# Kernel tuning notes

Hardware: AMD Instinct MI355X
Metric: run time of the kernel (lower is better)

## Reference

```python
import jax, jax.numpy as jnp
import numpy as np

B, N, S, C_IN = 8, 1024, 64, 1
H = 32  # hidden_ch


def _mpnn(W, b, x, g):
    # Faithful to MPNN(concat_h=False): messages[b,c,m,n] = x[b,c,m] * g[b,n,m],
    # flattened to (c m) channels and hit by a 1x1 conv W of shape (H, c, m).
    # out[b,u,n] = sum_{c,m} W[u,c,m] * x[b,c,m] * g[b,n,m] + b[u]
    t = jnp.einsum('ucm,bcm->bum', W, x)          # tiny contraction over c
    return jnp.einsum('bum,bnm->bun', t, g) + b[None, :, None]


def setup_inputs() -> dict:
    key = jax.random.key(0)
    ks = jax.random.split(key, 14)
    gate_scale = 1.0 / np.sqrt(C_IN * N)

    def gate_w(k):
        return jax.random.normal(k, (H, C_IN, N), jnp.float32) * gate_scale

    return {
        'x': jax.random.normal(ks[0], (B, N, S, C_IN), jnp.float32),
        'mask': jnp.ones((B, N, S, C_IN), dtype=bool),  # unused by the module
        'fwd_graph': jax.random.uniform(ks[1], (B, N, N), jnp.float32),
        # GRU gate MPNN 1x1-conv weights, reshaped (H, C_IN*N, 1) -> (H, C_IN, N)
        'Wf': gate_w(ks[2]), 'bf': jnp.zeros((H,), jnp.float32),
        'Wu': gate_w(ks[3]), 'bu': jnp.zeros((H,), jnp.float32),
        'Wc': gate_w(ks[4]), 'bc': jnp.zeros((H,), jnp.float32),
        'h0': jnp.zeros((H, N), jnp.float32),
        'W1': jax.random.normal(ks[5], (H, H), jnp.float32) / np.sqrt(H),
        'b1': jnp.zeros((H,), jnp.float32),
        'W2': jax.random.normal(ks[6], (H, 2 * H), jnp.float32) / np.sqrt(2 * H),
        'b2': jnp.zeros((H,), jnp.float32),
        # LocalConv1D: per-node 1x1 conv, weights (n, out_ch, 2H), bias (n, out_ch)
        'Wd': jax.random.normal(ks[7], (N, C_IN, 2 * H), jnp.float32) / np.sqrt(2 * H),
        'bd': jnp.zeros((N, C_IN), jnp.float32),
    }


def reference(x, mask, fwd_graph, Wf, bf, Wu, bu, Wc, bc, h0, W1, b1, W2, b2, Wd, bd):
    del mask  # present in the torch signature but never used
    b = x.shape[0]
    xs = jnp.transpose(x, (2, 0, 3, 1))  # (s, b, c, n)
    g = fwd_graph
    h_init = jnp.broadcast_to(h0[None], (b, H, N))

    def step(h, x_t):
        # NOTE: with concat_h=False the forget gate r = sigmoid(MPNN_f(x)) only
        # rescales h passed into c_gate, which ignores h entirely -> r (Wf, bf)
        # has no effect on the output; omitted here (same math).
        u = jax.nn.sigmoid(_mpnn(Wu, bu, x_t, g))
        c = jnp.tanh(_mpnn(Wc, bc, x_t, g))
        h_new = u * h + (1.0 - u) * c
        return h_new, None

    h, _ = jax.lax.scan(step, h_init, xs)

    # Prediction head (only the last step's prediction is returned: pred[:, :, -1:])
    x1 = jax.nn.leaky_relu(jnp.einsum('uh,bhn->bun', W1, h) + b1[None, :, None])
    x2 = jax.nn.leaky_relu(
        jnp.einsum('uk,bkn->bun', W2, jnp.concatenate([x1, h], axis=1)) + b2[None, :, None])
    dec_in = jnp.concatenate([x2, h], axis=1)  # (b, 2H, n)
    # LocalConv1D (per-node weights), fully batched:
    x_hat = jnp.einsum('nok,bkn->bon', Wd, dec_in) + bd.T[None, :, :]  # (b, c, n)
    return jnp.transpose(x_hat, (0, 2, 1))[:, :, None, :]  # (b, n, 1, c)
```

## Files before the change

kernel.cpp:

```cpp
#include <hip/hip_runtime.h>
#include <hip/hip_bf16.h>
#include <hip/hip_fp16.h>

#define Bsz 8
#define Nn 1024
#define Ss 64
#define Hh 32

typedef _Float16 half8 __attribute__((ext_vector_type(8)));
typedef _Float16 half4 __attribute__((ext_vector_type(4)));
typedef float f32x4 __attribute__((ext_vector_type(4)));

__device__ __forceinline__ void gload_lds16(const _Float16* g, _Float16* l) {
  __builtin_amdgcn_global_load_lds(
      (const __attribute__((address_space(1))) unsigned int*)g,
      (__attribute__((address_space(3))) unsigned int*)l, 16, 0, 0);
}

__global__ __launch_bounds__(256)
void prep(const float* __restrict__ x, const float* __restrict__ Wu,
          const float* __restrict__ Wc, const float* __restrict__ g,
          _Float16* __restrict__ xT, _Float16* __restrict__ Wh,
          _Float16* __restrict__ gh) {
  const int tid = threadIdx.x;
  if (blockIdx.x < 64) {
    const int b = blockIdx.x >> 3;
    const int m0 = (blockIdx.x & 7) * 128;
    __shared__ _Float16 tile[128 * 68];
    const int m = tid >> 1;
    const int hf = tid & 1;
    const float* src = x + ((size_t)(b * Nn + m0 + m)) * Ss + hf * 32;
#pragma unroll
    for (int i = 0; i < 8; ++i) {
      const float4 v = *(const float4*)(src + i * 4);
      half4 o;
      o[0] = (_Float16)v.x; o[1] = (_Float16)v.y;
      o[2] = (_Float16)v.z; o[3] = (_Float16)v.w;
      *(half4*)(&tile[m * 68 + hf * 32 + i * 4]) = o;
    }
    __syncthreads();
    const int t = tid & 63;
    const int q = tid >> 6;
    _Float16* dst = xT + ((size_t)(b * 64 + t)) * Nn + m0 + q * 32;
#pragma unroll
    for (int i = 0; i < 4; ++i) {
      half8 o;
#pragma unroll
      for (int e = 0; e < 8; ++e) o[e] = tile[(q * 32 + i * 8 + e) * 68 + t];
      *(half8*)(dst + i * 8) = o;
    }
  } else if (blockIdx.x < 72) {
    const int w = blockIdx.x - 64;
    const size_t i0 = ((size_t)(w * 256 + tid)) * 32;
#pragma unroll
    for (int i = 0; i < 8; ++i) {
      const size_t i4 = i0 + i * 4;
      const float* s = (i4 < 32768) ? (Wu + i4) : (Wc + (i4 - 32768));
      const float4 v = *(const float4*)s;
      half4 o;
      o[0] = (_Float16)v.x; o[1] = (_Float16)v.y;
      o[2] = (_Float16)v.z; o[3] = (_Float16)v.w;
      *(half4*)(&Wh[i4]) = o;
    }
  } else {
    const size_t i = ((size_t)(blockIdx.x - 72) * 256 + tid) * 4;
    const float4 v = *(const float4*)(&g[i]);
    half4 o;
    o[0] = (_Float16)v.x; o[1] = (_Float16)v.y;
    o[2] = (_Float16)v.z; o[3] = (_Float16)v.w;
    *(half4*)(&gh[i]) = o;
  }
}

__global__ __launch_bounds__(256)
void gemm_recur(const _Float16* __restrict__ xT, const _Float16* __restrict__ Wh,
                const _Float16* __restrict__ G, const float* __restrict__ bu,
                const float* __restrict__ bc, const float* __restrict__ h0,
                float* __restrict__ H) {
  __shared__ __align__(16) char smem[12288];
  _Float16* Xs = (_Float16*)smem;
  _Float16* Gs = (_Float16*)(smem + 4096);

  const int id = blockIdx.x;
  const int wg = (id & 7) * 256 + (id >> 3);
  const int b = wg >> 8;
  const int u = wg & 31;
  const int col0 = ((wg >> 5) & 7) * 128;

  const int tid = threadIdx.x;
  const int lane = tid & 63;
  const int wave = tid >> 6;
  const int wc = wave * 32;
  const int l15 = lane & 15;
  const int s = lane >> 4;

  const _Float16* Xb = xT + (size_t)b * 64 * Nn;
  const _Float16* Gb = G + ((size_t)b * Nn + col0) * Nn;
  const _Float16* Wg0 = Wh + (size_t)u * Nn;
  const _Float16* Wg1 = Wh + (size_t)(32 + u) * Nn;

  const int srow = lane >> 2;
  const int ssw = ((lane & 3) ^ ((lane >> 3) & 3)) * 8;
  const int ps8 = (s ^ ((l15 >> 1) & 3)) * 8;

  f32x4 acc[8][2] = {};

  for (int kk = 0; kk < 32; ++kk) {
    const int k0 = kk * 32;
    gload_lds16(Xb + (size_t)(wave * 16 + srow) * Nn + k0 + ssw,
                Xs + wave * 512);
    gload_lds16(Gb + (size_t)(wave * 32 + srow) * Nn + k0 + ssw,
                Gs + wave * 1024);
    gload_lds16(Gb + (size_t)(wave * 32 + 16 + srow) * Nn + k0 + ssw,
                Gs + wave * 1024 + 512);
    const half8 wv0 = *(const half8*)(Wg0 + k0 + s * 8);
    const half8 wv1 = *(const half8*)(Wg1 + k0 + s * 8);
    __syncthreads();

    half8 xf[4], bf[2];
#pragma unroll
    for (int q = 0; q < 4; ++q)
      xf[q] = *(const half8*)(&Xs[(q * 16 + l15) * 32 + ps8]);
#pragma unroll
    for (int ni = 0; ni < 2; ++ni)
      bf[ni] = *(const half8*)(&Gs[(wc + ni * 16 + l15) * 32 + ps8]);
#pragma unroll
    for (int mi = 0; mi < 8; ++mi) {
      const half8 af = xf[mi & 3] * (mi < 4 ? wv0 : wv1);
#pragma unroll
      for (int ni = 0; ni < 2; ++ni)
        acc[mi][ni] = __builtin_amdgcn_mfma_f32_16x16x32_f16(af, bf[ni], acc[mi][ni], 0, 0, 0);
    }
    __syncthreads();
  }

  const float bias_u = bu[u];
  const float bias_c = bc[u];
#pragma unroll
  for (int ni = 0; ni < 2; ++ni) {
    float At = 1.f, Bt = 0.f;
#pragma unroll
    for (int mi = 0; mi < 4; ++mi) {
      float A = 1.f, B = 0.f;
#pragma unroll
      for (int j = 0; j < 4; ++j) {
        const float yu = acc[mi][ni][j] + bias_u;
        const float yc = acc[mi + 4][ni][j] + bias_c;
        const float ug = 1.f / (1.f + __expf(-yu));
        const float e = __expf(-2.f * fabsf(yc));
        float th = (1.f - e) / (1.f + e);
        th = yc < 0.f ? -th : th;
        const float bj = (1.f - ug) * th;
        B = ug * B + bj;
        A = ug * A;
      }
      float Aall = __shfl(A, l15, 64);
      float Ball = __shfl(B, l15, 64);
#pragma unroll
      for (int sp = 1; sp < 4; ++sp) {
        const float As = __shfl(A, sp * 16 + l15, 64);
        const float Bs = __shfl(B, sp * 16 + l15, 64);
        Ball = As * Ball + Bs;
        Aall = As * Aall;
      }
      Bt = Aall * Bt + Ball;
      At = Aall * At;
    }
    if (s == (ni << 1)) {
      const int n = col0 + wc + ni * 16 + l15;
      const float hv = At * h0[u * Nn + n] + Bt;
      H[((size_t)b * Hh + u) * Nn + n] = hv;
    }
  }
}

__global__ __launch_bounds__(128)
void head(const float* __restrict__ H, const float* __restrict__ W1,
          const float* __restrict__ b1, const float* __restrict__ W2,
          const float* __restrict__ b2, const float* __restrict__ Wd,
          const float* __restrict__ bd, float* __restrict__ out) {
  const int b = blockIdx.x >> 3;
  const int n = (blockIdx.x & 7) * 128 + threadIdx.x;
  const float* Hb = H + (size_t)b * Hh * Nn;
  float h[32];
#pragma unroll
  for (int u = 0; u < 32; ++u) h[u] = Hb[u * Nn + n];
  float x1[32];
#pragma unroll 4
  for (int v = 0; v < 32; ++v) {
    float a = b1[v];
#pragma unroll
    for (int u = 0; u < 32; ++u) a += W1[v * 32 + u] * h[u];
    x1[v] = a > 0.f ? a : 0.01f * a;
  }
  float x2[32];
#pragma unroll 4
  for (int v = 0; v < 32; ++v) {
    float a = b2[v];
#pragma unroll
    for (int u = 0; u < 32; ++u) a += W2[v * 64 + u] * x1[u];
#pragma unroll
    for (int u = 0; u < 32; ++u) a += W2[v * 64 + 32 + u] * h[u];
    x2[v] = a > 0.f ? a : 0.01f * a;
  }
  float o = bd[n];
#pragma unroll
  for (int v = 0; v < 32; ++v) o += Wd[n * 64 + v] * x2[v];
#pragma unroll
  for (int v = 0; v < 32; ++v) o += Wd[n * 64 + 32 + v] * h[v];
  out[(size_t)b * Nn + n] = o;
}

extern "C" void kernel_launch(void* const* d_in, const int* in_sizes, int n_in,
                              void* d_out, int out_size, void* d_ws, size_t ws_size,
                              hipStream_t stream) {
  const float* x  = (const float*)d_in[0];
  const float* g  = (const float*)d_in[2];
  const float* Wu = (const float*)d_in[5];
  const float* bu = (const float*)d_in[6];
  const float* Wc = (const float*)d_in[7];
  const float* bc = (const float*)d_in[8];
  const float* h0 = (const float*)d_in[9];
  const float* W1 = (const float*)d_in[10];
  const float* b1 = (const float*)d_in[11];
  const float* W2 = (const float*)d_in[12];
  const float* b2 = (const float*)d_in[13];
  const float* Wd = (const float*)d_in[14];
  const float* bd = (const float*)d_in[15];
  float* out = (float*)d_out;

  char* ws = (char*)d_ws;
  _Float16* xT = (_Float16*)(ws);
  _Float16* Wh = (_Float16*)(ws + (size_t)(1u << 20));
  _Float16* gh = (_Float16*)(ws + (size_t)(2u << 20));
  float*    Hx = (float*)  (ws + (size_t)(18u << 20));

  prep<<<72 + 8192, 256, 0, stream>>>(x, Wu, Wc, g, xT, Wh, gh);
  gemm_recur<<<2048, 256, 0, stream>>>(xT, Wh, gh, bu, bc, h0, Hx);
  head<<<64, 128, 0, stream>>>(Hx, W1, b1, W2, b2, Wd, bd, out);
}
```

Baseline: 225.7 us.

## Double-buffer LDS tiles with async prefetch and stage gate weights in LDS

Converts the K loop of the recurrence GEMM to a double-buffered pipeline. The next X/G tile is issued via global_load_lds before the current tile is computed, with manual vmcnt waits and raw s_barriers in place of two __syncthreads. The Wu/Wc rows are loaded once into LDS instead of from global memory every iteration. The weight scaling is moved from the X fragments (8 multiplies) to the G fragments (4 multiplies). LDS usage grows from 12 KB to 28 KB, which can lower occupancy, and the hand-written waitcnt logic is fragile.

```diff
diff --git a/kernel.cpp b/kernel.cpp
--- a/kernel.cpp
+++ b/kernel.cpp
@@ -77,9 +77,12 @@
                 const _Float16* __restrict__ G, const float* __restrict__ bu,
                 const float* __restrict__ bc, const float* __restrict__ h0,
                 float* __restrict__ H) {
-  __shared__ __align__(16) char smem[12288];
-  _Float16* Xs = (_Float16*)smem;
-  _Float16* Gs = (_Float16*)(smem + 4096);
+  __shared__ __align__(16) char smem[28672];
+  _Float16* X0 = (_Float16*)smem;
+  _Float16* G0 = (_Float16*)(smem + 4096);
+  _Float16* X1 = (_Float16*)(smem + 12288);
+  _Float16* G1 = (_Float16*)(smem + 16384);
+  _Float16* Ws = (_Float16*)(smem + 24576);
 
   const int id = blockIdx.x;
   const int wg = (id & 7) * 256 + (id >> 3);
@@ -96,8 +99,6 @@
 
   const _Float16* Xb = xT + (size_t)b * 64 * Nn;
   const _Float16* Gb = G + ((size_t)b * Nn + col0) * Nn;
-  const _Float16* Wg0 = Wh + (size_t)u * Nn;
-  const _Float16* Wg1 = Wh + (size_t)(32 + u) * Nn;
 
   const int srow = lane >> 2;
   const int ssw = ((lane & 3) ^ ((lane >> 3) & 3)) * 8;
@@ -105,34 +106,65 @@
 
   f32x4 acc[8][2] = {};
 
+#define STAGE(k0s, Xd, Gd)                                                     \
+  do {                                                                         \
+    gload_lds16(Xb + (size_t)(wave * 16 + srow) * Nn + (k0s) + ssw,            \
+                (Xd) + wave * 512);                                            \
+    gload_lds16(Gb + (size_t)(wave * 32 + srow) * Nn + (k0s) + ssw,            \
+                (Gd) + wave * 1024);                                           \
+    gload_lds16(Gb + (size_t)(wave * 32 + 16 + srow) * Nn + (k0s) + ssw,       \
+                (Gd) + wave * 1024 + 512);                                     \
+  } while (0)
+
+  gload_lds16(Wh + (size_t)(wave >> 1) * 32768 + (size_t)u * Nn +
+                  ((wave & 1) * 512) + lane * 8,
+              Ws + (wave >> 1) * 1024 + (wave & 1) * 512);
+  STAGE(0, X0, G0);
+  __syncthreads();
+
+  const _Float16 *Xc = X0, *Gc = G0, *Xn = X1, *Gn = G1;
   for (int kk = 0; kk < 32; ++kk) {
+    if (kk < 31) {
+      STAGE((kk + 1) * 32, (_Float16*)Xn, (_Float16*)Gn);
+      asm volatile("s_waitcnt vmcnt(3)" ::: "memory");
+    } else {
+      asm volatile("s_waitcnt vmcnt(0)" ::: "memory");
+    }
+    __builtin_amdgcn_sched_barrier(0);
+    __builtin_amdgcn_s_barrier();
+    __builtin_amdgcn_sched_barrier(0);
+
     const int k0 = kk * 32;
-    gload_lds16(Xb + (size_t)(wave * 16 + srow) * Nn + k0 + ssw,
-                Xs + wave * 512);
-    gload_lds16(Gb + (size_t)(wave * 32 + srow) * Nn + k0 + ssw,
-                Gs + wave * 1024);
-    gload_lds16(Gb + (size_t)(wave * 32 + 16 + srow) * Nn + k0 + ssw,
-                Gs + wave * 1024 + 512);
-    const half8 wv0 = *(const half8*)(Wg0 + k0 + s * 8);
-    const half8 wv1 = *(const half8*)(Wg1 + k0 + s * 8);
-    __syncthreads();
-
-    half8 xf[4], bf[2];
+    const half8 wv0 = *(const half8*)(Ws + k0 + s * 8);
+    const half8 wv1 = *(const half8*)(Ws + 1024 + k0 + s * 8);
+    half8 xf[4], bf0[2], bf1[2];
 #pragma unroll
     for (int q = 0; q < 4; ++q)
-      xf[q] = *(const half8*)(&Xs[(q * 16 + l15) * 32 + ps8]);
-#pragma unroll
-    for (int ni = 0; ni < 2; ++ni)
-      bf[ni] = *(const half8*)(&Gs[(wc + ni * 16 + l15) * 32 + ps8]);
-#pragma unroll
-    for (int mi = 0; mi < 8; ++mi) {
-      const half8 af = xf[mi & 3] * (mi < 4 ? wv0 : wv1);
+      xf[q] = *(const half8*)(&Xc[(q * 16 + l15) * 32 + ps8]);
+#pragma unroll
+    for (int ni = 0; ni < 2; ++ni) {
+      const half8 gr = *(const half8*)(&Gc[(wc + ni * 16 + l15) * 32 + ps8]);
+      bf0[ni] = gr * wv0;
+      bf1[ni] = gr * wv1;
+    }
+#pragma unroll
+    for (int mi = 0; mi < 4; ++mi)
 #pragma unroll
       for (int ni = 0; ni < 2; ++ni)
-        acc[mi][ni] = __builtin_amdgcn_mfma_f32_16x16x32_f16(af, bf[ni], acc[mi][ni], 0, 0, 0);
-    }
-    __syncthreads();
-  }
+        acc[mi][ni] = __builtin_amdgcn_mfma_f32_16x16x32_f16(xf[mi], bf0[ni], acc[mi][ni], 0, 0, 0);
+#pragma unroll
+    for (int mi = 0; mi < 4; ++mi)
+#pragma unroll
+      for (int ni = 0; ni < 2; ++ni)
+        acc[mi + 4][ni] = __builtin_amdgcn_mfma_f32_16x16x32_f16(xf[mi], bf1[ni], acc[mi + 4][ni], 0, 0, 0);
+
+    __builtin_amdgcn_sched_barrier(0);
+    __builtin_amdgcn_s_barrier();
+    const _Float16* tp;
+    tp = Xc; Xc = Xn; Xn = tp;
+    tp = Gc; Gc = Gn; Gn = tp;
+  }
+#undef STAGE
 
   const float bias_u = bu[u];
   const float bias_c = bc[u];
```

Result: no change. 227.4 us (+0.8%).
